# Optimization experiments

Hardware: AMD Instinct MI355X
Metric: run time of the kernel (lower is better)

The kernel has to match this reference:

```python
import jax, jax.numpy as jnp
import numpy as np

LAMBDA_COORD = 5.0
LAMBDA_NOOBJ = 0.5
CELL_SILE = 1.0 / 7.0


def setup_inputs() -> dict:
    key = jax.random.key(0)
    k1, k2, k3 = jax.random.split(key, 3)
    B, S, C = 16384, 49, 30
    predictions = jax.random.normal(k1, (B, S, C), dtype=jnp.float32)
    targets = jax.random.uniform(k2, (B, S, C), dtype=jnp.float32)
    # confidence column must be exactly 0/1 for the equality masks in the loss
    obj = (jax.random.uniform(k3, (B, S)) < 0.3).astype(jnp.float32)
    targets = targets.at[:, :, 4].set(obj)
    return {"predictions": predictions, "targets": targets}


def reference(predictions, targets):
    # Flatten cells: row-major order matches torch boolean indexing order.
    p = predictions.reshape(-1, 30)  # [N, 30], N = B*49
    t = targets.reshape(-1, 30)
    conf = t[:, 4]
    coord_mask = conf == 1.0
    noobj = (conf == 0.0).astype(p.dtype)

    # no-object confidence loss on columns [4, 9]
    noobj_loss = LAMBDA_NOOBJ * jnp.sum(
        noobj * ((p[:, 4] - t[:, 4]) ** 2 + (p[:, 9] - t[:, 9]) ** 2))

    # The original zips N_obj rows against N_obj//2 output rows, so only the
    # first floor(N_obj/2) object cells (in flattened order) contribute.
    n_obj = jnp.sum(coord_mask.astype(jnp.int32))
    rank = jnp.cumsum(coord_mask.astype(jnp.int32))  # 1-indexed object rank
    w = (coord_mask & (rank <= n_obj // 2)).astype(p.dtype)

    # pred boxes: columns [0:4] and [5:9] -> [N, 2, 4]
    pb = p[:, :10].reshape(-1, 2, 5)[..., :4]
    # faithful in-place transform: a = xy*c - wh ; b = a*c + wh
    pa = pb[..., :2] * CELL_SILE - pb[..., 2:4]
    pbb = pa * CELL_SILE + pb[..., 2:4]
    pbox = jnp.concatenate([pa, pbb], axis=-1)  # [N, 2, 4]

    tb = jnp.square(t[:, :4])
    ta = tb[:, :2] * CELL_SILE - tb[:, 2:4]
    tbb = ta * CELL_SILE + tb[:, 2:4]
    tbox = jnp.concatenate([ta, tbb], axis=-1)  # [N, 4]

    # torchvision.ops.box_iou, batched over cells
    lt = jnp.maximum(pbox[..., :2], tbox[:, None, :2])
    rb = jnp.minimum(pbox[..., 2:], tbox[:, None, 2:])
    whd = jnp.clip(rb - lt, 0.0)
    inter = whd[..., 0] * whd[..., 1]  # [N, 2]
    area_p = (pbox[..., 2] - pbox[..., 0]) * (pbox[..., 3] - pbox[..., 1])
    area_t = (tbox[:, 2] - tbox[:, 0]) * (tbox[:, 3] - tbox[:, 1])
    iou = inter / (area_p + area_t[:, None] - inter)  # [N, 2]

    idx = jnp.argmax(iou, axis=1)  # responsible box per cell
    sel = jnp.take_along_axis(p[:, :10].reshape(-1, 2, 5),
                              idx[:, None, None], axis=1)[:, 0, :]  # [N, 5]
    obj_idx = jnp.argmax(t[:, 10:], axis=1)
    sel_cls = jnp.take_along_axis(p[:, 10:], obj_idx[:, None], axis=1)[:, 0]

    center = jnp.sum(w * jnp.sum((sel[:, :2] - t[:, :2]) ** 2, axis=1))
    xywh = jnp.sum(w * jnp.sum((sel[:, 2:4] - t[:, 2:4]) ** 2, axis=1))
    # original compares column 5 twice (confidence_loss and classier_loss are
    # the same term): pred class prob vs constant 1
    conf_l = jnp.sum(w * (sel_cls - 1.0) ** 2)
    cls_l = jnp.sum(w * (sel_cls - 1.0) ** 2)

    return LAMBDA_COORD * (center + xywh + conf_l + cls_l) + noobj_loss
```

## Files before the change

### kernel.cpp

```cpp
#include <hip/hip_runtime.h>


#define COLS 30
#define NB   3136

__device__ __forceinline__ void row_load_compute(
    const float* __restrict__ gp, const float* __restrict__ gt, long row,
    bool& coord, float& r, float& noo)
{
    const float2* P2 = (const float2*)(gp + row * (long)COLS);
    const float2* T2 = (const float2*)(gt + row * (long)COLS);
    float2 a0 = P2[0],  a1 = P2[1],  a2 = P2[2],  a3 = P2[3],  a4 = P2[4];
    float2 a5 = P2[5],  a6 = P2[6],  a7 = P2[7],  a8 = P2[8],  a9 = P2[9];
    float2 a10 = P2[10], a11 = P2[11], a12 = P2[12], a13 = P2[13], a14 = P2[14];
    float2 b0 = T2[0],  b1 = T2[1],  b2 = T2[2],  b3 = T2[3],  b4 = T2[4];
    float2 b5 = T2[5],  b6 = T2[6],  b7 = T2[7],  b8 = T2[8],  b9 = T2[9];
    float2 b10 = T2[10], b11 = T2[11], b12 = T2[12], b13 = T2[13], b14 = T2[14];

    const float C = 1.0f / 7.0f;
    float conf = b2.x;
    coord = (conf == 1.0f);
    noo = 0.0f;
    if (conf == 0.0f) {
        float d4 = a2.x - conf;
        float d9 = a4.y - b4.y;
        noo = d4 * d4 + d9 * d9;
    }
    float T0 = b0.x, T1 = b0.y, T2v = b1.x, T3 = b1.y;
    float tb0 = T0 * T0, tb1 = T1 * T1, tb2 = T2v * T2v, tb3 = T3 * T3;
    float tax = tb0 * C - tb2, tay = tb1 * C - tb3;
    float tbx = tax * C + tb2, tby = tay * C + tb3;
    float areaT = (tbx - tax) * (tby - tay);
    float pax0 = a0.x * C - a1.x, pay0 = a0.y * C - a1.y;
    float pbx0 = pax0 * C + a1.x, pby0 = pay0 * C + a1.y;
    float pax1 = a2.y * C - a3.y, pay1 = a3.x * C - a4.x;
    float pbx1 = pax1 * C + a3.y, pby1 = pay1 * C + a4.x;
    float ltx = fmaxf(pax0, tax), lty = fmaxf(pay0, tay);
    float rbx = fminf(pbx0, tbx), rby = fminf(pby0, tby);
    float wx = fmaxf(rbx - ltx, 0.0f), wy = fmaxf(rby - lty, 0.0f);
    float inter = wx * wy;
    float areaP = (pbx0 - pax0) * (pby0 - pay0);
    float iou0 = inter / (areaP + areaT - inter);
    ltx = fmaxf(pax1, tax); lty = fmaxf(pay1, tay);
    rbx = fminf(pbx1, tbx); rby = fminf(pby1, tby);
    wx = fmaxf(rbx - ltx, 0.0f); wy = fmaxf(rby - lty, 0.0f);
    inter = wx * wy;
    areaP = (pbx1 - pax1) * (pby1 - pay1);
    float iou1 = inter / (areaP + areaT - inter);

    int idx = (iou1 > iou0) ? 1 : 0;
    float sx = idx ? a2.y : a0.x;
    float sy = idx ? a3.x : a0.y;
    float sw = idx ? a3.y : a1.x;
    float sh = idx ? a4.x : a1.y;
    float best = b5.x, pc = a5.x;
#define CLS_STEP(tv, pv) { float v_ = (tv); if (v_ > best) { best = v_; pc = (pv); } }
    CLS_STEP(b5.y,  a5.y)  CLS_STEP(b6.x,  a6.x)  CLS_STEP(b6.y,  a6.y)
    CLS_STEP(b7.x,  a7.x)  CLS_STEP(b7.y,  a7.y)  CLS_STEP(b8.x,  a8.x)
    CLS_STEP(b8.y,  a8.y)  CLS_STEP(b9.x,  a9.x)  CLS_STEP(b9.y,  a9.y)
    CLS_STEP(b10.x, a10.x) CLS_STEP(b10.y, a10.y) CLS_STEP(b11.x, a11.x)
    CLS_STEP(b11.y, a11.y) CLS_STEP(b12.x, a12.x) CLS_STEP(b12.y, a12.y)
    CLS_STEP(b13.x, a13.x) CLS_STEP(b13.y, a13.y) CLS_STEP(b14.x, a14.x)
    CLS_STEP(b14.y, a14.y)
#undef CLS_STEP
    float d0 = sx - T0, d1 = sy - T1, d2 = sw - T2v, d3 = sh - T3;
    float dc = pc - 1.0f;
    r = d0 * d0 + d1 * d1 + d2 * d2 + d3 * d3 + 2.0f * dc * dc;
}

__global__ __launch_bounds__(256, 4) void yolo_k1(const float* __restrict__ gp,
                                                  const float* __restrict__ gt,
                                                  int* __restrict__ cnt,
                                                  float* __restrict__ sumR,
                                                  float* __restrict__ noo) {
    __shared__ float wr[4], wn[4];
    __shared__ int wc[4];
    int tid = threadIdx.x;
    long row = (long)blockIdx.x * 256 + tid;
    bool coord; float r, nt;
    row_load_compute(gp, gt, row, coord, r, nt);
    float rl = coord ? r : 0.0f;

    unsigned long long bal = __ballot(coord);
    int c = (int)__popcll(bal);
#pragma unroll
    for (int off = 32; off > 0; off >>= 1) {
        rl += __shfl_down(rl, off);
        nt += __shfl_down(nt, off);
    }
    int wave = tid >> 6, lane = tid & 63;
    if (lane == 0) { wr[wave] = rl; wn[wave] = nt; wc[wave] = c; }
    __syncthreads();
    if (tid == 0) {
        cnt[blockIdx.x]  = wc[0] + wc[1] + wc[2] + wc[3];
        sumR[blockIdx.x] = wr[0] + wr[1] + wr[2] + wr[3];
        noo[blockIdx.x]  = wn[0] + wn[1] + wn[2] + wn[3];
    }
}

__global__ __launch_bounds__(256) void yolo_k2(const int* __restrict__ cnt,
                                               const float* __restrict__ sumR,
                                               const float* __restrict__ noo,
                                               const float* __restrict__ gp,
                                               const float* __restrict__ gt,
                                               float* __restrict__ out) {
    __shared__ int   wsum[4];
    __shared__ float wf[4], wn2[4];
    __shared__ int   s_bstar, s_kstar;
    __shared__ float s_base;
    __shared__ int   s_wcnt[4];
    int tid = threadIdx.x;
    int lane = tid & 63, wave = tid >> 6;
    if (tid == 0) { s_bstar = -1; s_kstar = 0; }

    const int PER = 13;
    int start = tid * PER;
    int end = min(NB, start + PER);

    int cloc = 0; float nloc = 0.0f;
    for (int i = start; i < end; ++i) { cloc += cnt[i]; nloc += noo[i]; }

    int incl = cloc;
#pragma unroll
    for (int off = 1; off < 64; off <<= 1) {
        int v = __shfl_up(incl, off);
        if (lane >= off) incl += v;
    }
    if (lane == 63) wsum[wave] = incl;
    __syncthreads();
    int woff = 0;
#pragma unroll
    for (int w = 0; w < 4; ++w) woff += (w < wave) ? wsum[w] : 0;
    int ex = woff + incl - cloc;
    int n_obj = wsum[0] + wsum[1] + wsum[2] + wsum[3];
    int n_half = n_obj >> 1;

    float acc = 0.0f;
    int running = ex;
    for (int i = start; i < end; ++i) {
        int ci = cnt[i];
        if (ci > 0) {
            if (running + ci <= n_half) {
                acc += sumR[i];
            } else if (running < n_half) {
                s_bstar = i;
                s_kstar = n_half - running;
            }
        }
        running += ci;
    }

#pragma unroll
    for (int off = 32; off > 0; off >>= 1) {
        acc  += __shfl_down(acc, off);
        nloc += __shfl_down(nloc, off);
    }
    if (lane == 0) { wf[wave] = acc; wn2[wave] = nloc; }
    __syncthreads();
    if (tid == 0)
        s_base = 5.0f * (wf[0] + wf[1] + wf[2] + wf[3])
               + 0.5f * (wn2[0] + wn2[1] + wn2[2] + wn2[3]);
    __syncthreads();

    int bstar = s_bstar, kstar = s_kstar;
    float total = 0.0f;
    if (bstar >= 0) {
        long row = (long)bstar * 256 + tid;
        bool coord; float r, nt;
        row_load_compute(gp, gt, row, coord, r, nt);
        unsigned long long bal = __ballot(coord);
        if (lane == 0) s_wcnt[wave] = (int)__popcll(bal);
        __syncthreads();
        int waveoff = 0;
#pragma unroll
        for (int w = 0; w < 4; ++w) waveoff += (w < wave) ? s_wcnt[w] : 0;
        unsigned long long below_incl =
            (lane == 63) ? bal : (bal & ((1ull << (lane + 1)) - 1ull));
        int rank = waveoff + (int)__popcll(below_incl);
        float val = (coord && rank <= kstar) ? r : 0.0f;
#pragma unroll
        for (int off = 32; off > 0; off >>= 1) val += __shfl_down(val, off);
        if (lane == 0) wf[wave] = val;
        __syncthreads();
        if (tid == 0) total = wf[0] + wf[1] + wf[2] + wf[3];
    }
    if (tid == 0) out[0] = s_base + 5.0f * total;
}

extern "C" void kernel_launch(void* const* d_in, const int* in_sizes, int n_in,
                              void* d_out, int out_size, void* d_ws, size_t ws_size,
                              hipStream_t stream) {
    (void)in_sizes; (void)n_in; (void)out_size; (void)ws_size;
    const float* p = (const float*)d_in[0];
    const float* t = (const float*)d_in[1];
    char* ws = (char*)d_ws;
    int*   cnt  = (int*)ws;
    float* sumR = (float*)(ws + (size_t)NB * 4);
    float* noo  = (float*)(ws + (size_t)NB * 8);
    float* out  = (float*)d_out;

    yolo_k1<<<NB, 256, 0, stream>>>(p, t, cnt, sumR, noo);
    yolo_k2<<<1, 256, 0, stream>>>(cnt, sumR, noo, p, t, out);
}
```

Baseline: 215.8 us.

## Stream row tiles into LDS with double-buffered async global_load_lds in persistent blocks

Replaces the one-row-per-thread kernel with a persistent grid of 512 single-wave blocks. Each block walks 128-row tiles and stages predictions and targets into LDS through double-buffered global_load_lds. It waits on vmcnt so the next tile's load overlaps compute on the current one, and writes packed per-tile stats as float4. The aim is a coalesced, streamed read of the roughly 190MB input in place of strided 120-byte-per-thread float2 loads. The risk is that only 512 waves of 64 threads may not generate enough memory parallelism to saturate HBM on a 256-CU part, and the LDS row reads with a 30-float stride may bank-conflict.

After: 219.7 us. No clear change (+1.8%).

```diff
diff --git a/kernel.cpp b/kernel.cpp
--- a/kernel.cpp
+++ b/kernel.cpp
@@ -2,14 +2,15 @@
 
 
 #define COLS 30
-#define NB   3136
-
-__device__ __forceinline__ void row_load_compute(
-    const float* __restrict__ gp, const float* __restrict__ gt, long row,
+#define TROWS 128
+#define TBYTES (TROWS * COLS * 4)
+#define NT2 6272
+#define GRID1 512
+
+__device__ __forceinline__ void row_compute_f2(
+    const float2* __restrict__ P2, const float2* __restrict__ T2,
     bool& coord, float& r, float& noo)
 {
-    const float2* P2 = (const float2*)(gp + row * (long)COLS);
-    const float2* T2 = (const float2*)(gt + row * (long)COLS);
     float2 a0 = P2[0],  a1 = P2[1],  a2 = P2[2],  a3 = P2[3],  a4 = P2[4];
     float2 a5 = P2[5],  a6 = P2[6],  a7 = P2[7],  a8 = P2[8],  a9 = P2[9];
     float2 a10 = P2[10], a11 = P2[11], a12 = P2[12], a13 = P2[13], a14 = P2[14];
@@ -68,39 +69,69 @@
     r = d0 * d0 + d1 * d1 + d2 * d2 + d3 * d3 + 2.0f * dc * dc;
 }
 
-__global__ __launch_bounds__(256, 4) void yolo_k1(const float* __restrict__ gp,
-                                                  const float* __restrict__ gt,
-                                                  int* __restrict__ cnt,
-                                                  float* __restrict__ sumR,
-                                                  float* __restrict__ noo) {
-    __shared__ float wr[4], wn[4];
-    __shared__ int wc[4];
+__device__ __forceinline__ void stage_tile(const float* __restrict__ gp,
+                                           const float* __restrict__ gt,
+                                           float* lbuf, long tile, int tid) {
+    const char* gpb = (const char*)gp + tile * (long)TBYTES;
+    const char* gtb = (const char*)gt + tile * (long)TBYTES;
+    char* lb = (char*)lbuf;
+    asm volatile("" ::: "memory");
+#pragma unroll
+    for (int r = 0; r < 15; ++r) {
+        int off = r * 1024 + tid * 16;
+        __builtin_amdgcn_global_load_lds(
+            (const __attribute__((address_space(1))) void*)(gpb + off),
+            (__attribute__((address_space(3))) void*)(lb + off), 16, 0, 0);
+    }
+#pragma unroll
+    for (int r = 0; r < 15; ++r) {
+        int off = r * 1024 + tid * 16;
+        __builtin_amdgcn_global_load_lds(
+            (const __attribute__((address_space(1))) void*)(gtb + off),
+            (__attribute__((address_space(3))) void*)(lb + TBYTES + off), 16, 0, 0);
+    }
+    asm volatile("" ::: "memory");
+}
+
+__global__ __launch_bounds__(64, 1) void yolo_k1(const float* __restrict__ gp,
+                                                 const float* __restrict__ gt,
+                                                 float4* __restrict__ stats) {
+    __shared__ float buf[2][2 * TROWS * COLS];
     int tid = threadIdx.x;
-    long row = (long)blockIdx.x * 256 + tid;
-    bool coord; float r, nt;
-    row_load_compute(gp, gt, row, coord, r, nt);
-    float rl = coord ? r : 0.0f;
-
-    unsigned long long bal = __ballot(coord);
-    int c = (int)__popcll(bal);
-#pragma unroll
-    for (int off = 32; off > 0; off >>= 1) {
-        rl += __shfl_down(rl, off);
-        nt += __shfl_down(nt, off);
-    }
-    int wave = tid >> 6, lane = tid & 63;
-    if (lane == 0) { wr[wave] = rl; wn[wave] = nt; wc[wave] = c; }
-    __syncthreads();
-    if (tid == 0) {
-        cnt[blockIdx.x]  = wc[0] + wc[1] + wc[2] + wc[3];
-        sumR[blockIdx.x] = wr[0] + wr[1] + wr[2] + wr[3];
-        noo[blockIdx.x]  = wn[0] + wn[1] + wn[2] + wn[3];
-    }
-}
-
-__global__ __launch_bounds__(256) void yolo_k2(const int* __restrict__ cnt,
-                                               const float* __restrict__ sumR,
-                                               const float* __restrict__ noo,
+    int bid = blockIdx.x;
+    int ntiles = 12 + (bid < (NT2 - GRID1 * 12) ? 1 : 0);
+
+    stage_tile(gp, gt, buf[0], bid, tid);
+    for (int j = 0; j < ntiles; ++j) {
+        long tile = (long)bid + (long)j * GRID1;
+        int cur = j & 1;
+        bool has_next = (j + 1 < ntiles);
+        if (has_next)
+            stage_tile(gp, gt, buf[cur ^ 1], (long)bid + (long)(j + 1) * GRID1, tid);
+        if (has_next) asm volatile("s_waitcnt vmcnt(30)" ::: "memory");
+        else          asm volatile("s_waitcnt vmcnt(0)"  ::: "memory");
+
+        const float* lp = buf[cur];
+        const float* lt = buf[cur] + TROWS * COLS;
+        bool cA, cB; float rA, rB, nA, nB;
+        row_compute_f2((const float2*)(lp + tid * COLS),
+                       (const float2*)(lt + tid * COLS), cA, rA, nA);
+        row_compute_f2((const float2*)(lp + (tid + 64) * COLS),
+                       (const float2*)(lt + (tid + 64) * COLS), cB, rB, nB);
+        float rl = (cA ? rA : 0.0f) + (cB ? rB : 0.0f);
+        float nn = nA + nB;
+        int c = (int)__popcll(__ballot(cA)) + (int)__popcll(__ballot(cB));
+#pragma unroll
+        for (int off = 32; off > 0; off >>= 1) {
+            rl += __shfl_down(rl, off);
+            nn += __shfl_down(nn, off);
+        }
+        if (tid == 0) stats[tile] = make_float4((float)c, rl, nn, 0.0f);
+        asm volatile("" ::: "memory");
+    }
+}
+
+__global__ __launch_bounds__(256) void yolo_k2(const float4* __restrict__ stats,
                                                const float* __restrict__ gp,
                                                const float* __restrict__ gt,
                                                float* __restrict__ out) {
@@ -113,12 +144,15 @@
     int lane = tid & 63, wave = tid >> 6;
     if (tid == 0) { s_bstar = -1; s_kstar = 0; }
 
-    const int PER = 13;
+    const int PER = 25;
     int start = tid * PER;
-    int end = min(NB, start + PER);
+    int end = min(NT2, start + PER);
 
     int cloc = 0; float nloc = 0.0f;
-    for (int i = start; i < end; ++i) { cloc += cnt[i]; nloc += noo[i]; }
+    for (int i = start; i < end; ++i) {
+        float4 s = stats[i];
+        cloc += (int)s.x; nloc += s.z;
+    }
 
     int incl = cloc;
 #pragma unroll
@@ -138,10 +172,11 @@
     float acc = 0.0f;
     int running = ex;
     for (int i = start; i < end; ++i) {
-        int ci = cnt[i];
+        float4 s = stats[i];
+        int ci = (int)s.x;
         if (ci > 0) {
             if (running + ci <= n_half) {
-                acc += sumR[i];
+                acc += s.y;
             } else if (running < n_half) {
                 s_bstar = i;
                 s_kstar = n_half - running;
@@ -165,9 +200,14 @@
     int bstar = s_bstar, kstar = s_kstar;
     float total = 0.0f;
     if (bstar >= 0) {
-        long row = (long)bstar * 256 + tid;
-        bool coord; float r, nt;
-        row_load_compute(gp, gt, row, coord, r, nt);
+        bool coord = false; float r = 0.0f;
+        if (tid < TROWS) {
+            long row = (long)bstar * TROWS + tid;
+            float nthrow;
+            row_compute_f2((const float2*)(gp + row * (long)COLS),
+                           (const float2*)(gt + row * (long)COLS),
+                           coord, r, nthrow);
+        }
         unsigned long long bal = __ballot(coord);
         if (lane == 0) s_wcnt[wave] = (int)__popcll(bal);
         __syncthreads();
@@ -193,12 +233,9 @@
     (void)in_sizes; (void)n_in; (void)out_size; (void)ws_size;
     const float* p = (const float*)d_in[0];
     const float* t = (const float*)d_in[1];
-    char* ws = (char*)d_ws;
-    int*   cnt  = (int*)ws;
-    float* sumR = (float*)(ws + (size_t)NB * 4);
-    float* noo  = (float*)(ws + (size_t)NB * 8);
-    float* out  = (float*)d_out;
-
-    yolo_k1<<<NB, 256, 0, stream>>>(p, t, cnt, sumR, noo);
-    yolo_k2<<<1, 256, 0, stream>>>(cnt, sumR, noo, p, t, out);
-}
+    float4* stats = (float4*)d_ws;
+    float* out = (float*)d_out;
+
+    yolo_k1<<<GRID1, 64, 0, stream>>>(p, t, stats);
+    yolo_k2<<<1, 256, 0, stream>>>(stats, p, t, out);
+}
```
